# Kernel optimization log

Measured on AMD Instinct MI355X. Metric: run time of the kernel, lower is better.

Reference implementation:

```python
import jax, jax.numpy as jnp
import numpy as np

B, D, N, H = 4, 512, 1536, 8
DIM = D // H  # per-head dim = 64


def _conv1x1(x, w, b):
    # Conv1d(kernel_size=1): x [B, C, N], w [O, C], b [O]
    return jnp.einsum('oc,bcn->bon', w, x) + b[None, :, None]


def setup_inputs() -> dict:
    key = jax.random.key(0)
    ks = jax.random.split(key, 13)
    s = 0.02
    return {
        'query': jax.random.normal(ks[0], (B, D, N), jnp.float32),
        'key': jax.random.normal(ks[1], (B, D, N), jnp.float32),
        'value': jax.random.normal(ks[2], (B, D, N), jnp.float32),
        'dist': jax.random.uniform(ks[3], (B, N, N), jnp.float32),
        'mask': jax.random.bernoulli(ks[4], 0.9, (N, N)),  # bool [N, M]
        'Wq': jax.random.normal(ks[5], (D, D), jnp.float32) * s,
        'bq': jnp.zeros((D,), jnp.float32),
        'Wk': jax.random.normal(ks[6], (D, D), jnp.float32) * s,
        'bk': jnp.zeros((D,), jnp.float32),
        'Wv': jax.random.normal(ks[7], (D, D), jnp.float32) * s,
        'bv': jnp.zeros((D,), jnp.float32),
        'Wm': jax.random.normal(ks[8], (D, D), jnp.float32) * s,
        'bm': jnp.zeros((D,), jnp.float32),
    }


def reference(query, key, value, dist, mask, Wq, bq, Wk, bk, Wv, bv, Wm, bm):
    # dist is accepted but unused, exactly as in the original forward.
    q = _conv1x1(query, Wq, bq).reshape(B, DIM, H, N)
    k = _conv1x1(key, Wk, bk).reshape(B, DIM, H, N)
    v = _conv1x1(value, Wv, bv).reshape(B, DIM, H, N)
    scores = jnp.einsum('bdhn,bdhm->bhnm', q, k) / jnp.sqrt(jnp.float32(DIM))
    # custom additive mask: (detached global min - 20) on masked-out positions
    pen = (jax.lax.stop_gradient(scores.min()) - 20.0) * (~mask).astype(scores.dtype)
    scores = scores + pen[None, None]  # broadcast over [B, H]
    prob = jax.nn.softmax(scores, axis=-1)
    x = jnp.einsum('bhnm,bdhm->bdhn', prob, v).reshape(B, D, N)
    out = _conv1x1(x, Wm, bm)
    return out, scores.mean(axis=1)
```

## Files before the change

### kernel.cpp

```cpp
#include <hip/hip_runtime.h>
#include <hip/hip_bf16.h>

typedef __hip_bfloat16 bf16;
typedef __attribute__((ext_vector_type(8))) short s16x8;
typedef __attribute__((ext_vector_type(4))) float f32x4;
typedef unsigned char uchar;

#define B_   4
#define D_   512
#define N_   1536
#define H_   8
#define DIM_ 64
#define NN_  (N_*N_)

#define MFMA(a,b,c) __builtin_amdgcn_mfma_f32_16x16x32_bf16((a),(b),(c),0,0,0)

__device__ __forceinline__ short b16(float x){ bf16 h = __float2bfloat16(x); return *reinterpret_cast<short*>(&h); }
__device__ __forceinline__ float f16f(short s){ bf16 h = *reinterpret_cast<bf16*>(&s); return __bfloat162float(h); }

__device__ __forceinline__ s16x8 w8(const float* p){
  float4 u = *(const float4*)p, v = *(const float4*)(p+4);
  s16x8 r;
  r[0]=b16(u.x); r[1]=b16(u.y); r[2]=b16(u.z); r[3]=b16(u.w);
  r[4]=b16(v.x); r[5]=b16(v.y); r[6]=b16(v.z); r[7]=b16(v.w);
  return r;
}

__device__ unsigned detect_w4(const uchar* __restrict__ mraw, int* sh, int t){
  if (t == 0){ sh[0] = 0; sh[1] = 0; }
  __syncthreads();
  int a = 0, bb = 0;
  for (int i = t; i < 4096; i += 256){
    uchar v = mraw[i];
    if (v > 1) a = 1;
    else if (v && (i & 3)) bb = 1;
  }
  if (a)  atomicOr(&sh[0], 1);
  if (bb) atomicOr(&sh[1], 1);
  __syncthreads();
  return sh[0] ? 1u : (sh[1] ? 0u : 1u);
}

__global__ void detect_k(const uchar* __restrict__ mraw, unsigned* __restrict__ flags){
  __shared__ int sh[2];
  unsigned w4 = detect_w4(mraw, sh, threadIdx.x);
  if (threadIdx.x == 0) flags[0] = w4;
}

__global__ __launch_bounds__(256) void cvtW_k(const float* __restrict__ W0, const float* __restrict__ W1,
                                              const float* __restrict__ W2, const float* __restrict__ W3,
                                              bf16* __restrict__ dst){
  const float* src = (blockIdx.y==0)?W0:(blockIdx.y==1)?W1:(blockIdx.y==2)?W2:W3;
  bf16* d = dst + (size_t)blockIdx.y*(D_*D_);
  int i = (blockIdx.x*256 + threadIdx.x)*4;
  float4 v = *(const float4*)(src + i);
  __align__(8) short tmp[4] = {b16(v.x), b16(v.y), b16(v.z), b16(v.w)};
  *(int2*)((short*)d + i) = *(const int2*)tmp;
}

__device__ __forceinline__ void load_mt(uchar (*mt)[64], const void* mraw, unsigned w4,
                                        int n0, int m0, int t){
  int row = t >> 2, c = (t & 3) * 16;
  if (!w4){
    *(int4*)&mt[row][c] = *(const int4*)((const uchar*)mraw + (size_t)(n0 + row)*N_ + m0 + c);
  } else {
    const unsigned* mp = (const unsigned*)mraw + (size_t)(n0 + row)*N_ + m0 + c;
    uchar tmp[16];
    #pragma unroll
    for (int j = 0; j < 16; ++j) tmp[j] = mp[j] ? 1 : 0;
    *(int4*)&mt[row][c] = *(const int4*)tmp;
  }
}

__device__ __forceinline__ int mask_at(const void* mraw, unsigned w4, int n, int m){
  if (w4) return ((const unsigned*)mraw)[(size_t)n*N_ + m] != 0;
  return ((const uchar*)mraw)[(size_t)n*N_ + m] != 0;
}

template<int WBF>
__global__ __launch_bounds__(256) void convQKf_k(const float* __restrict__ X, const float* __restrict__ Wf,
                                                 const bf16* __restrict__ Wb,
                                                 const float* __restrict__ bias, bf16* __restrict__ dst,
                                                 float scale){
  int b = blockIdx.z, ot = blockIdx.y, nt = blockIdx.x;
  int t = threadIdx.x, w = t >> 6, L = t & 63, g = L >> 4, q = L & 15;
  __shared__ short Xs[64][72];
  __shared__ short tile[64][72];
  f32x4 acc[4] = {};
  float4 pf[4];
  #pragma unroll
  for (int it = 0; it < 4; ++it){
    int i = it*256 + t, cc = i >> 4, nq = (i & 15)*4;
    pf[it] = *(const float4*)(X + ((size_t)b*D_ + cc)*N_ + nt*64 + nq);
  }
  for (int cs = 0; cs < 8; ++cs){
    __syncthreads();
    #pragma unroll
    for (int it = 0; it < 4; ++it){
      int i = it*256 + t, cc = i >> 4, nq = (i & 15)*4;
      Xs[nq+0][cc] = b16(pf[it].x); Xs[nq+1][cc] = b16(pf[it].y);
      Xs[nq+2][cc] = b16(pf[it].z); Xs[nq+3][cc] = b16(pf[it].w);
    }
    if (cs < 7){
      #pragma unroll
      for (int it = 0; it < 4; ++it){
        int i = it*256 + t, cc = i >> 4, nq = (i & 15)*4;
        pf[it] = *(const float4*)(X + ((size_t)b*D_ + (cs+1)*64 + cc)*N_ + nt*64 + nq);
      }
    }
    __syncthreads();
    #pragma unroll
    for (int kk = 0; kk < 64; kk += 32){
      s16x8 a = *(const s16x8*)&Xs[w*16 + q][kk + 8*g];
      #pragma unroll
      for (int f = 0; f < 4; ++f){
        s16x8 bb;
        if (WBF) bb = *(const s16x8*)(Wb + (size_t)(ot*64 + f*16 + q)*D_ + cs*64 + kk + 8*g);
        else     bb = w8(Wf + (size_t)(ot*64 + f*16 + q)*D_ + cs*64 + kk + 8*g);
        acc[f] = MFMA(a, bb, acc[f]);
      }
    }
  }
  #pragma unroll
  for (int f = 0; f < 4; ++f){
    float bv = bias[ot*64 + f*16 + q];
    #pragma unroll
    for (int r = 0; r < 4; ++r)
      tile[w*16 + 4*g + r][f*16 + q] = b16((acc[f][r] + bv)*scale);
  }
  __syncthreads();
  #pragma unroll
  for (int it = 0; it < 2; ++it){
    int s = t + 256*it, row = s >> 3, h = s & 7;
    short tmp[8];
    #pragma unroll
    for (int j = 0; j < 8; ++j) tmp[j] = tile[row][h + 8*j];
    *(int4*)((short*)dst + ((size_t)(b*8+h)*N_ + nt*64 + row)*DIM_ + ot*8) = *(const int4*)tmp;
  }
}

template<int WBF>
__global__ __launch_bounds__(256) void convVf_k(const float* __restrict__ X, const float* __restrict__ Wf,
                                                const bf16* __restrict__ Wb,
                                                const float* __restrict__ bias, bf16* __restrict__ dst){
  int b = blockIdx.z, ot = blockIdx.y, nt = blockIdx.x;
  int t = threadIdx.x, w = t >> 6, L = t & 63, g = L >> 4, q = L & 15;
  __shared__ short Xs[64][72];
  __shared__ short tile[64][72];
  f32x4 acc[4] = {};
  float4 pf[4];
  #pragma unroll
  for (int it = 0; it < 4; ++it){
    int i = it*256 + t, cc = i >> 4, nq = (i & 15)*4;
    pf[it] = *(const float4*)(X + ((size_t)b*D_ + cc)*N_ + nt*64 + nq);
  }
  for (int cs = 0; cs < 8; ++cs){
    __syncthreads();
    #pragma unroll
    for (int it = 0; it < 4; ++it){
      int i = it*256 + t, cc = i >> 4, nq = (i & 15)*4;
      Xs[nq+0][cc] = b16(pf[it].x); Xs[nq+1][cc] = b16(pf[it].y);
      Xs[nq+2][cc] = b16(pf[it].z); Xs[nq+3][cc] = b16(pf[it].w);
    }
    if (cs < 7){
      #pragma unroll
      for (int it = 0; it < 4; ++it){
        int i = it*256 + t, cc = i >> 4, nq = (i & 15)*4;
        pf[it] = *(const float4*)(X + ((size_t)b*D_ + (cs+1)*64 + cc)*N_ + nt*64 + nq);
      }
    }
    __syncthreads();
    #pragma unroll
    for (int kk = 0; kk < 64; kk += 32){
      s16x8 a = *(const s16x8*)&Xs[w*16 + q][kk + 8*g];
      #pragma unroll
      for (int f = 0; f < 4; ++f){
        s16x8 bb;
        if (WBF) bb = *(const s16x8*)(Wb + (size_t)(ot*64 + f*16 + q)*D_ + cs*64 + kk + 8*g);
        else     bb = w8(Wf + (size_t)(ot*64 + f*16 + q)*D_ + cs*64 + kk + 8*g);
        acc[f] = MFMA(a, bb, acc[f]);
      }
    }
  }
  #pragma unroll
  for (int f = 0; f < 4; ++f){
    float bv = bias[ot*64 + f*16 + q];
    #pragma unroll
    for (int r = 0; r < 4; ++r)
      tile[w*16 + 4*g + r][f*16 + q] = b16(acc[f][r] + bv);
  }
  __syncthreads();
  int col = t & 63, seg = t >> 6;
  int h = col & 7, d = ot*8 + (col >> 3);
  short tmp[16];
  #pragma unroll
  for (int j = 0; j < 16; ++j) tmp[j] = tile[seg*16 + j][col];
  short* p = (short*)dst + ((size_t)(b*8+h)*DIM_ + d)*N_ + nt*64 + seg*16;
  *(int4*)p       = *(const int4*)&tmp[0];
  *(int4*)(p + 8) = *(const int4*)&tmp[8];
}

__global__ __launch_bounds__(256) void passA_k(const bf16* __restrict__ QH, const bf16* __restrict__ KH,
                                               float* __restrict__ out2f, float* __restrict__ bmin){
  int b = blockIdx.z, ntb = blockIdx.y, mtb = blockIdx.x;
  int t = threadIdx.x, w = t >> 6, L = t & 63, g = L >> 4, q = L & 15;
  __shared__ short Ks[2][64][72];
  int r0 = t >> 3, s0 = (t & 7)*8, r1 = (t + 256) >> 3;
  f32x4 mean[4] = {};
  float vmin = 3.4e38f;
  {
    const bf16* kb = KH + ((size_t)(b*H_)*N_ + mtb*64)*DIM_;
    *(int4*)&Ks[0][r0][s0] = *(const int4*)(kb + (size_t)r0*DIM_ + s0);
    *(int4*)&Ks[0][r1][s0] = *(const int4*)(kb + (size_t)r1*DIM_ + s0);
  }
  const bf16* qrow0 = QH + ((size_t)(b*H_)*N_ + ntb*64 + w*16 + q)*DIM_;
  s16x8 qa0 = *(const s16x8*)(qrow0 + 8*g);
  s16x8 qa1 = *(const s16x8*)(qrow0 + 32 + 8*g);
  int4 kn0, kn1; s16x8 qn0, qn1;
  {
    const bf16* kb = KH + ((size_t)(b*H_ + 1)*N_ + mtb*64)*DIM_;
    kn0 = *(const int4*)(kb + (size_t)r0*DIM_ + s0);
    kn1 = *(const int4*)(kb + (size_t)r1*DIM_ + s0);
    const bf16* qrow = QH + ((size_t)(b*H_ + 1)*N_ + ntb*64 + w*16 + q)*DIM_;
    qn0 = *(const s16x8*)(qrow + 8*g);
    qn1 = *(const s16x8*)(qrow + 32 + 8*g);
  }
  __syncthreads();
  for (int h = 0; h < H_; ++h){
    f32x4 acc[4] = {};
    #pragma unroll
    for (int f = 0; f < 4; ++f){
      acc[f] = MFMA(qa0, *(const s16x8*)&Ks[h&1][f*16 + q][8*g], acc[f]);
      acc[f] = MFMA(qa1, *(const s16x8*)&Ks[h&1][f*16 + q][32 + 8*g], acc[f]);
    }
    if (h < H_-1){
      *(int4*)&Ks[(h+1)&1][r0][s0] = kn0;
      *(int4*)&Ks[(h+1)&1][r1][s0] = kn1;
      qa0 = qn0; qa1 = qn1;
      if (h < H_-2){
        const bf16* kb = KH + ((size_t)(b*H_ + h+2)*N_ + mtb*64)*DIM_;
        kn0 = *(const int4*)(kb + (size_t)r0*DIM_ + s0);
        kn1 = *(const int4*)(kb + (size_t)r1*DIM_ + s0);
        const bf16* qrow = QH + ((size_t)(b*H_ + h+2)*N_ + ntb*64 + w*16 + q)*DIM_;
        qn0 = *(const s16x8*)(qrow + 8*g);
        qn1 = *(const s16x8*)(qrow + 32 + 8*g);
      }
    }
    #pragma unroll
    for (int f = 0; f < 4; ++f){
      #pragma unroll
      for (int r = 0; r < 4; ++r) vmin = fminf(vmin, acc[f][r]);
      mean[f] += acc[f];
    }
    __syncthreads();
  }
  #pragma unroll
  for (int off = 32; off; off >>= 1) vmin = fminf(vmin, __shfl_xor(vmin, off));
  __shared__ float wmin[4];
  if (L == 0) wmin[w] = vmin;
  __syncthreads();
  if (t == 0)
    bmin[((size_t)b*24 + ntb)*24 + mtb] = fminf(fminf(wmin[0],wmin[1]), fminf(wmin[2],wmin[3]));
  #pragma unroll
  for (int f = 0; f < 4; ++f)
    #pragma unroll
    for (int r = 0; r < 4; ++r)
      out2f[(size_t)b*NN_ + (size_t)(ntb*64 + w*16 + 4*g + r)*N_ + mtb*64 + f*16 + q]
        = mean[f][r] * 0.125f;
}

__global__ void minred_k(const float* __restrict__ bmin, float* __restrict__ penp){
  int t = threadIdx.x;
  float m = 3.4e38f;
  for (int i = t; i < 2304; i += 256) m = fminf(m, bmin[i]);
  #pragma unroll
  for (int off = 32; off; off >>= 1) m = fminf(m, __shfl_xor(m, off));
  __shared__ float wm[4];
  if ((t & 63) == 0) wm[t >> 6] = m;
  __syncthreads();
  if (t == 0) penp[0] = fminf(fminf(wm[0],wm[1]), fminf(wm[2],wm[3])) - 20.0f;
}

__global__ __launch_bounds__(256) void passCf_k(const void* __restrict__ mraw,
                                                const unsigned* __restrict__ flags,
                                                const float* __restrict__ penp,
                                                float* __restrict__ out2f){
  int i = blockIdx.x*256 + threadIdx.x;
  if (i >= NN_) return;
  int keep = flags[0] ? (((const unsigned*)mraw)[i] != 0) : (((const uchar*)mraw)[i] != 0);
  if (keep) return;
  float pen = penp[0];
  #pragma unroll
  for (int b = 0; b < B_; ++b) out2f[(size_t)b*NN_ + i] += pen;
}

__global__ __launch_bounds__(256) void passBs_k(const bf16* __restrict__ QH, const bf16* __restrict__ KH,
                                                const bf16* __restrict__ VT, const void* __restrict__ mraw,
                                                const unsigned* __restrict__ flags,
                                                bf16* __restrict__ Opart, float* __restrict__ lpart){
  int z = blockIdx.z, half = z >> 2, b = z & 3;
  int h = blockIdx.y, ntb = blockIdx.x;
  int t = threadIdx.x, w = t >> 6, L = t & 63, g = L >> 4, q = L & 15;
  __shared__ short Ks[64][72], Vs[64][72];
  __shared__ uchar mt[64][64];
  __shared__ short P[4][16][72];
  unsigned w4 = flags[0];
  size_t bh = (size_t)(b*H_ + h);
  const bf16* kbase = KH + bh*N_*DIM_;
  const bf16* vbase = VT + bh*(size_t)DIM_*N_;
  const bf16* qrow = QH + (bh*N_ + ntb*64 + w*16 + q)*DIM_;
  s16x8 qa0 = *(const s16x8*)(qrow + 8*g);
  s16x8 qa1 = *(const s16x8*)(qrow + 32 + 8*g);
  int r0 = t >> 3, s0 = (t & 7)*8, r1 = (t + 256) >> 3;
  int mrow = t >> 2, mc = (t & 3)*16;
  int4 kreg0, kreg1, vreg0, vreg1, mreg4[4];
  float lacc[4] = {0.f,0.f,0.f,0.f};
  f32x4 O[4] = {};
  int mt0 = half*12;
  {
    int m0 = mt0*64;
    kreg0 = *(const int4*)(kbase + (size_t)(m0 + r0)*DIM_ + s0);
    kreg1 = *(const int4*)(kbase + (size_t)(m0 + r1)*DIM_ + s0);
    vreg0 = *(const int4*)(vbase + (size_t)r0*N_ + m0 + s0);
    vreg1 = *(const int4*)(vbase + (size_t)r1*N_ + m0 + s0);
    if (!w4) mreg4[0] = *(const int4*)((const uchar*)mraw + (size_t)(ntb*64 + mrow)*N_ + m0 + mc);
    else {
      const int4* mp = (const int4*)((const unsigned*)mraw + (size_t)(ntb*64 + mrow)*N_ + m0 + mc);
      #pragma unroll
      for (int j = 0; j < 4; ++j) mreg4[j] = mp[j];
    }
  }
  for (int i = 0; i < 12; ++i){
    __syncthreads();
    *(int4*)&Ks[r0][s0] = kreg0;
    *(int4*)&Ks[r1][s0] = kreg1;
    *(int4*)&Vs[r0][s0] = vreg0;
    *(int4*)&Vs[r1][s0] = vreg1;
    if (!w4) *(int4*)&mt[mrow][mc] = mreg4[0];
    else {
      uchar tmp[16];
      #pragma unroll
      for (int j = 0; j < 16; ++j) tmp[j] = ((const unsigned*)mreg4)[j] ? 1 : 0;
      *(int4*)&mt[mrow][mc] = *(const int4*)tmp;
    }
    if (i < 11){
      int m0 = (mt0 + i + 1)*64;
      kreg0 = *(const int4*)(kbase + (size_t)(m0 + r0)*DIM_ + s0);
      kreg1 = *(const int4*)(kbase + (size_t)(m0 + r1)*DIM_ + s0);
      vreg0 = *(const int4*)(vbase + (size_t)r0*N_ + m0 + s0);
      vreg1 = *(const int4*)(vbase + (size_t)r1*N_ + m0 + s0);
      if (!w4) mreg4[0] = *(const int4*)((const uchar*)mraw + (size_t)(ntb*64 + mrow)*N_ + m0 + mc);
      else {
        const int4* mp = (const int4*)((const unsigned*)mraw + (size_t)(ntb*64 + mrow)*N_ + m0 + mc);
        #pragma unroll
        for (int j = 0; j < 4; ++j) mreg4[j] = mp[j];
      }
    }
    __syncthreads();
    f32x4 acc[4] = {};
    #pragma unroll
    for (int f = 0; f < 4; ++f){
      acc[f] = MFMA(qa0, *(const s16x8*)&Ks[f*16 + q][8*g], acc[f]);
      acc[f] = MFMA(qa1, *(const s16x8*)&Ks[f*16 + q][32 + 8*g], acc[f]);
    }
    float pv[4][4];
    #pragma unroll
    for (int f = 0; f < 4; ++f)
      #pragma unroll
      for (int r = 0; r < 4; ++r)
        pv[f][r] = mt[w*16 + 4*g + r][f*16 + q] ? __expf(acc[f][r]) : 0.0f;
    #pragma unroll
    for (int r = 0; r < 4; ++r)
      lacc[r] += (pv[0][r] + pv[1][r]) + (pv[2][r] + pv[3][r]);
    #pragma unroll
    for (int f = 0; f < 4; ++f)
      #pragma unroll
      for (int r = 0; r < 4; ++r)
        P[w][4*g + r][f*16 + q] = b16(pv[f][r]);
    #pragma unroll
    for (int f2 = 0; f2 < 4; ++f2){
      O[f2] = MFMA(*(const s16x8*)&P[w][q][8*g],      *(const s16x8*)&Vs[f2*16 + q][8*g],      O[f2]);
      O[f2] = MFMA(*(const s16x8*)&P[w][q][32 + 8*g], *(const s16x8*)&Vs[f2*16 + q][32 + 8*g], O[f2]);
    }
  }
  #pragma unroll
  for (int r = 0; r < 4; ++r){
    #pragma unroll
    for (int off = 1; off < 16; off <<= 1) lacc[r] += __shfl_xor(lacc[r], off);
  }
  bf16* Op = Opart + (size_t)half*((size_t)B_*H_*N_*DIM_);
  float* lp = lpart + (size_t)half*((size_t)B_*H_*N_);
  if (q == 0){
    #pragma unroll
    for (int r = 0; r < 4; ++r)
      lp[bh*N_ + ntb*64 + w*16 + 4*g + r] = lacc[r];
  }
  #pragma unroll
  for (int f2 = 0; f2 < 4; ++f2)
    #pragma unroll
    for (int r = 0; r < 4; ++r){
      int n = ntb*64 + w*16 + 4*g + r, d = f2*16 + q;
      ((short*)Op)[(bh*N_ + n)*DIM_ + d] = b16(O[f2][r]);
    }
}

__global__ __launch_bounds__(256) void merge_k(const bf16* __restrict__ Opart, const float* __restrict__ lpart,
                                               bf16* __restrict__ xT){
  int b = blockIdx.z, h = blockIdx.y, nt = blockIdx.x, t = threadIdx.x;
  int nl = t >> 3, d0 = (t & 7)*8;
  int n = nt*32 + nl;
  size_t bh = (size_t)(b*H_ + h);
  size_t row = bh*N_ + n;
  const size_t OS = (size_t)B_*H_*N_*DIM_, LS = (size_t)B_*H_*N_;
  float inv = 1.0f / (lpart[row] + lpart[LS + row]);
  int4 a = *(const int4*)((const short*)Opart + row*DIM_ + d0);
  int4 c = *(const int4*)((const short*)Opart + OS*1 + row*DIM_ + d0);
  const short* as = (const short*)&a;
  const short* cs = (const short*)&c;
  short* out = (short*)xT + ((size_t)b*N_ + n)*D_ + h;
  #pragma unroll
  for (int j = 0; j < 8; ++j)
    out[(size_t)(d0 + j)*8] = b16((f16f(as[j]) + f16f(cs[j])) * inv);
}

__global__ __launch_bounds__(256) void passB_k(const bf16* __restrict__ QH, const bf16* __restrict__ KH,
                                               const bf16* __restrict__ VT, const void* __restrict__ mraw,
                                               bf16* __restrict__ xT){
  int b = blockIdx.z, h = blockIdx.y, ntb = blockIdx.x;
  int t = threadIdx.x, w = t >> 6, L = t & 63, g = L >> 4, q = L & 15;
  __shared__ short Ks[64][72], Vs[64][72];
  __shared__ uchar mt[64][64];
  __shared__ short P[4][16][72];
  __shared__ int dsh[2];
  unsigned w4 = detect_w4((const uchar*)mraw, dsh, t);
  size_t bh = (size_t)(b*H_ + h);
  const bf16* kbase = KH + bh*N_*DIM_;
  const bf16* vbase = VT + bh*(size_t)DIM_*N_;
  const bf16* qrow = QH + (bh*N_ + ntb*64 + w*16 + q)*DIM_;
  s16x8 qa0 = *(const s16x8*)(qrow + 8*g);
  s16x8 qa1 = *(const s16x8*)(qrow + 32 + 8*g);
  int r0 = t >> 3, s0 = (t & 7)*8, r1 = (t + 256) >> 3;
  int mrow = t >> 2, mc = (t & 3)*16;
  int4 kreg0, kreg1, vreg0, vreg1, mreg4[4];
  float lacc[4] = {0.f,0.f,0.f,0.f};
  f32x4 O[4] = {};
  {
    kreg0 = *(const int4*)(kbase + (size_t)r0*DIM_ + s0);
    kreg1 = *(const int4*)(kbase + (size_t)r1*DIM_ + s0);
    vreg0 = *(const int4*)(vbase + (size_t)r0*N_ + s0);
    vreg1 = *(const int4*)(vbase + (size_t)r1*N_ + s0);
    if (!w4) mreg4[0] = *(const int4*)((const uchar*)mraw + (size_t)(ntb*64 + mrow)*N_ + mc);
    else {
      const int4* mp = (const int4*)((const unsigned*)mraw + (size_t)(ntb*64 + mrow)*N_ + mc);
      #pragma unroll
      for (int j = 0; j < 4; ++j) mreg4[j] = mp[j];
    }
  }
  for (int mtb = 0; mtb < 24; ++mtb){
    __syncthreads();
    *(int4*)&Ks[r0][s0] = kreg0;
    *(int4*)&Ks[r1][s0] = kreg1;
    *(int4*)&Vs[r0][s0] = vreg0;
    *(int4*)&Vs[r1][s0] = vreg1;
    if (!w4) *(int4*)&mt[mrow][mc] = mreg4[0];
    else {
      uchar tmp[16];
      #pragma unroll
      for (int j = 0; j < 16; ++j) tmp[j] = ((const unsigned*)mreg4)[j] ? 1 : 0;
      *(int4*)&mt[mrow][mc] = *(const int4*)tmp;
    }
    if (mtb < 23){
      int m0 = (mtb+1)*64;
      kreg0 = *(const int4*)(kbase + (size_t)(m0 + r0)*DIM_ + s0);
      kreg1 = *(const int4*)(kbase + (size_t)(m0 + r1)*DIM_ + s0);
      vreg0 = *(const int4*)(vbase + (size_t)r0*N_ + m0 + s0);
      vreg1 = *(const int4*)(vbase + (size_t)r1*N_ + m0 + s0);
      if (!w4) mreg4[0] = *(const int4*)((const uchar*)mraw + (size_t)(ntb*64 + mrow)*N_ + m0 + mc);
      else {
        const int4* mp = (const int4*)((const unsigned*)mraw + (size_t)(ntb*64 + mrow)*N_ + m0 + mc);
        #pragma unroll
        for (int j = 0; j < 4; ++j) mreg4[j] = mp[j];
      }
    }
    __syncthreads();
    f32x4 acc[4] = {};
    #pragma unroll
    for (int f = 0; f < 4; ++f){
      acc[f] = MFMA(qa0, *(const s16x8*)&Ks[f*16 + q][8*g], acc[f]);
      acc[f] = MFMA(qa1, *(const s16x8*)&Ks[f*16 + q][32 + 8*g], acc[f]);
    }
    float pv[4][4];
    #pragma unroll
    for (int f = 0; f < 4; ++f)
      #pragma unroll
      for (int r = 0; r < 4; ++r)
        pv[f][r] = mt[w*16 + 4*g + r][f*16 + q] ? __expf(acc[f][r]) : 0.0f;
    #pragma unroll
    for (int r = 0; r < 4; ++r)
      lacc[r] += (pv[0][r] + pv[1][r]) + (pv[2][r] + pv[3][r]);
    #pragma unroll
    for (int f = 0; f < 4; ++f)
      #pragma unroll
      for (int r = 0; r < 4; ++r)
        P[w][4*g + r][f*16 + q] = b16(pv[f][r]);
    #pragma unroll
    for (int f2 = 0; f2 < 4; ++f2){
      O[f2] = MFMA(*(const s16x8*)&P[w][q][8*g],      *(const s16x8*)&Vs[f2*16 + q][8*g],      O[f2]);
      O[f2] = MFMA(*(const s16x8*)&P[w][q][32 + 8*g], *(const s16x8*)&Vs[f2*16 + q][32 + 8*g], O[f2]);
    }
  }
  #pragma unroll
  for (int r = 0; r < 4; ++r){
    #pragma unroll
    for (int off = 1; off < 16; off <<= 1) lacc[r] += __shfl_xor(lacc[r], off);
  }
  float inv[4];
  #pragma unroll
  for (int r = 0; r < 4; ++r) inv[r] = 1.0f / lacc[r];
  #pragma unroll
  for (int f2 = 0; f2 < 4; ++f2)
    #pragma unroll
    for (int r = 0; r < 4; ++r){
      int n = ntb*64 + w*16 + 4*g + r, d = f2*16 + q;
      ((short*)xT)[((size_t)b*N_ + n)*D_ + d*8 + h] = b16(O[f2][r]*inv[r]);
    }
}

template<int WBF>
__global__ __launch_bounds__(256) void gemm2_k(const float* __restrict__ Wmf, const bf16* __restrict__ Wmb,
                                               const float* __restrict__ bm,
                                               const bf16* __restrict__ xT, float* __restrict__ out0f){
  int b = blockIdx.z, ot = blockIdx.y, nt = blockIdx.x;
  int t = threadIdx.x, w = t >> 6, L = t & 63, g = L >> 4, q = L & 15;
  f32x4 acc[4] = {};
  for (int kk = 0; kk < D_; kk += 32){
    s16x8 a;
    if (WBF) a = *(const s16x8*)(Wmb + (size_t)(ot*64 + w*16 + q)*D_ + kk + 8*g);
    else     a = w8(Wmf + (size_t)(ot*64 + w*16 + q)*D_ + kk + 8*g);
    #pragma unroll
    for (int f = 0; f < 4; ++f){
      s16x8 bb = *(const s16x8*)(xT + ((size_t)b*N_ + nt*64 + f*16 + q)*D_ + kk + 8*g);
      acc[f] = MFMA(a, bb, acc[f]);
    }
  }
  #pragma unroll
  for (int f = 0; f < 4; ++f)
    #pragma unroll
    for (int r = 0; r < 4; ++r){
      int o = ot*64 + w*16 + 4*g + r;
      out0f[((size_t)b*D_ + o)*N_ + nt*64 + f*16 + q] = acc[f][r] + bm[o];
    }
}

__global__ __launch_bounds__(256) void t64_k(const float* __restrict__ X, bf16* __restrict__ XT){
  int b = blockIdx.z, ct = blockIdx.y, nt = blockIdx.x, t = threadIdx.x;
  __shared__ bf16 T[64][72];
  #pragma unroll
  for (int it = 0; it < 4; ++it){
    int idx = t + 256*it, cc = idx >> 4, s = idx & 15;
    float4 v = *(const float4*)(X + ((size_t)b*D_ + ct*64 + cc)*N_ + nt*64 + s*4);
    T[cc][s*4+0] = __float2bfloat16(v.x);
    T[cc][s*4+1] = __float2bfloat16(v.y);
    T[cc][s*4+2] = __float2bfloat16(v.z);
    T[cc][s*4+3] = __float2bfloat16(v.w);
  }
  __syncthreads();
  #pragma unroll
  for (int it = 0; it < 2; ++it){
    int idx = t + 256*it, nn = idx >> 3, s = idx & 7;
    short tmp[8];
    #pragma unroll
    for (int j = 0; j < 8; ++j) tmp[j] = *(short*)&T[s*8 + j][nn];
    *(int4*)((short*)XT + ((size_t)b*N_ + nt*64 + nn)*D_ + ct*64 + s*8) = *(const int4*)tmp;
  }
}

__global__ __launch_bounds__(256) void convQK_k(const bf16* __restrict__ XT, const float* __restrict__ W,
                                                const float* __restrict__ bias, bf16* __restrict__ dst,
                                                float scale){
  int b = blockIdx.z, ot = blockIdx.y, nt = blockIdx.x;
  int t = threadIdx.x, w = t >> 6, L = t & 63, g = L >> 4, q = L & 15;
  const bf16* Arow = XT + ((size_t)b*N_ + nt*64 + w*16 + q)*D_;
  f32x4 acc[4] = {};
  for (int kk = 0; kk < D_; kk += 32){
    s16x8 a = *(const s16x8*)(Arow + kk + 8*g);
    #pragma unroll
    for (int f = 0; f < 4; ++f){
      s16x8 bb = w8(W + (size_t)(ot*64 + f*16 + q)*D_ + kk + 8*g);
      acc[f] = MFMA(a, bb, acc[f]);
    }
  }
  __shared__ short tile[64][72];
  #pragma unroll
  for (int f = 0; f < 4; ++f){
    float bv = bias[ot*64 + f*16 + q];
    #pragma unroll
    for (int r = 0; r < 4; ++r)
      tile[w*16 + 4*g + r][f*16 + q] = b16((acc[f][r] + bv)*scale);
  }
  __syncthreads();
  #pragma unroll
  for (int it = 0; it < 2; ++it){
    int s = t + 256*it, row = s >> 3, h = s & 7;
    short tmp[8];
    #pragma unroll
    for (int j = 0; j < 8; ++j) tmp[j] = tile[row][h + 8*j];
    *(int4*)((short*)dst + ((size_t)(b*8+h)*N_ + nt*64 + row)*DIM_ + ot*8) = *(const int4*)tmp;
  }
}

__global__ __launch_bounds__(256) void convV_k(const bf16* __restrict__ XT, const float* __restrict__ W,
                                               const float* __restrict__ bias, bf16* __restrict__ dst){
  int b = blockIdx.z, ot = blockIdx.y, nt = blockIdx.x;
  int t = threadIdx.x, w = t >> 6, L = t & 63, g = L >> 4, q = L & 15;
  const bf16* Arow = XT + ((size_t)b*N_ + nt*64 + w*16 + q)*D_;
  f32x4 acc[4] = {};
  for (int kk = 0; kk < D_; kk += 32){
    s16x8 a = *(const s16x8*)(Arow + kk + 8*g);
    #pragma unroll
    for (int f = 0; f < 4; ++f){
      s16x8 bb = w8(W + (size_t)(ot*64 + f*16 + q)*D_ + kk + 8*g);
      acc[f] = MFMA(a, bb, acc[f]);
    }
  }
  __shared__ short tile[64][72];
  #pragma unroll
  for (int f = 0; f < 4; ++f){
    float bv = bias[ot*64 + f*16 + q];
    #pragma unroll
    for (int r = 0; r < 4; ++r)
      tile[w*16 + 4*g + r][f*16 + q] = b16(acc[f][r] + bv);
  }
  __syncthreads();
  int col = t & 63, seg = t >> 6;
  int h = col & 7, d = ot*8 + (col >> 3);
  short tmp[16];
  #pragma unroll
  for (int j = 0; j < 16; ++j) tmp[j] = tile[seg*16 + j][col];
  short* p = (short*)dst + ((size_t)(b*8+h)*DIM_ + d)*N_ + nt*64 + seg*16;
  *(int4*)p       = *(const int4*)&tmp[0];
  *(int4*)(p + 8) = *(const int4*)&tmp[8];
}

__global__ __launch_bounds__(256) void min_k(const bf16* __restrict__ QH, const bf16* __restrict__ KH,
                                             float* __restrict__ bmin){
  int b = blockIdx.z, ntb = blockIdx.y, mtb = blockIdx.x;
  int t = threadIdx.x, w = t >> 6, L = t & 63, g = L >> 4, q = L & 15;
  float vmin = 3.4e38f;
  for (int h = 0; h < H_; ++h){
    size_t bh = (size_t)(b*H_ + h);
    const bf16* qrow = QH + (bh*N_ + ntb*64 + w*16 + q)*DIM_;
    const bf16* krow = KH + (bh*N_ + mtb*64 + q)*DIM_;
    f32x4 acc[4] = {};
    #pragma unroll
    for (int kk = 0; kk < 64; kk += 32){
      s16x8 a = *(const s16x8*)(qrow + kk + 8*g);
      #pragma unroll
      for (int f = 0; f < 4; ++f){
        s16x8 bb = *(const s16x8*)(krow + (size_t)f*16*DIM_ + kk + 8*g);
        acc[f] = MFMA(a, bb, acc[f]);
      }
    }
    #pragma unroll
    for (int f = 0; f < 4; ++f)
      #pragma unroll
      for (int r = 0; r < 4; ++r) vmin = fminf(vmin, acc[f][r]);
  }
  #pragma unroll
  for (int off = 32; off; off >>= 1) vmin = fminf(vmin, __shfl_xor(vmin, off));
  __shared__ float wmin[4];
  if (L == 0) wmin[w] = vmin;
  __syncthreads();
  if (t == 0)
    bmin[((size_t)b*24 + ntb)*24 + mtb] = fminf(fminf(wmin[0],wmin[1]), fminf(wmin[2],wmin[3]));
}

__global__ __launch_bounds__(256) void meanLow_k(const bf16* __restrict__ QH, const bf16* __restrict__ KH,
                                                 const void* __restrict__ mraw, const float* __restrict__ penp,
                                                 float* __restrict__ out2f){
  int mtb = blockIdx.x, rt = blockIdx.y;
  if (rt == 48 && mtb == 0) return;
  __shared__ uchar mt[64][64];
  __shared__ int dsh[2];
  int t = threadIdx.x, w = t >> 6, L = t & 63, g = L >> 4, q = L & 15;
  unsigned w4 = detect_w4((const uchar*)mraw, dsh, t);
  int gr = rt*64, b = gr / N_, n0 = gr % N_;
  load_mt(mt, mraw, w4, n0, mtb*64, t);
  __syncthreads();
  float pen = penp[0];
  f32x4 mean[4] = {};
  for (int h = 0; h < H_; ++h){
    size_t bh = (size_t)(b*H_ + h);
    const bf16* qrow = QH + (bh*N_ + n0 + w*16 + q)*DIM_;
    const bf16* krow = KH + (bh*N_ + mtb*64 + q)*DIM_;
    f32x4 acc[4] = {};
    #pragma unroll
    for (int kk = 0; kk < 64; kk += 32){
      s16x8 a = *(const s16x8*)(qrow + kk + 8*g);
      #pragma unroll
      for (int f = 0; f < 4; ++f){
        s16x8 bb = *(const s16x8*)(krow + (size_t)f*16*DIM_ + kk + 8*g);
        acc[f] = MFMA(a, bb, acc[f]);
      }
    }
    #pragma unroll
    for (int f = 0; f < 4; ++f) mean[f] += acc[f];
  }
  #pragma unroll
  for (int f = 0; f < 4; ++f)
    #pragma unroll
    for (int r = 0; r < 4; ++r){
      float v = mean[f][r]*0.125f;
      if (!mt[w*16 + 4*g + r][f*16 + q]) v += pen;
      out2f[(size_t)b*NN_ + (size_t)(n0 + w*16 + 4*g + r)*N_ + mtb*64 + f*16 + q] = v;
    }
}

__device__ void build_head(const float* __restrict__ X, const float* __restrict__ W,
                           const float* __restrict__ bias, int b, int n0, int h,
                           short (*dst)[72], short (*Xs)[72], int t){
  int w = t >> 6, L = t & 63, g = L >> 4, q = L & 15;
  f32x4 acc[4] = {};
  for (int cs = 0; cs < 8; ++cs){
    __syncthreads();
    #pragma unroll
    for (int it = 0; it < 4; ++it){
      int i = it*256 + t, cc = i >> 4, nq = (i & 15)*4;
      float4 v = *(const float4*)(X + ((size_t)b*D_ + cs*64 + cc)*N_ + n0 + nq);
      Xs[nq+0][cc] = b16(v.x); Xs[nq+1][cc] = b16(v.y);
      Xs[nq+2][cc] = b16(v.z); Xs[nq+3][cc] = b16(v.w);
    }
    __syncthreads();
    #pragma unroll
    for (int kk = 0; kk < 64; kk += 32){
      s16x8 a = w8(W + (size_t)((w*16 + q)*8 + h)*D_ + cs*64 + kk + 8*g);
      #pragma unroll
      for (int f = 0; f < 4; ++f){
        s16x8 bb = *(const s16x8*)&Xs[f*16 + q][kk + 8*g];
        acc[f] = MFMA(a, bb, acc[f]);
      }
    }
  }
  __syncthreads();
  #pragma unroll
  for (int f = 0; f < 4; ++f)
    #pragma unroll
    for (int r = 0; r < 4; ++r){
      int d = w*16 + 4*g + r, n = f*16 + q;
      dst[n][d] = b16(acc[f][r] + bias[d*8 + h]);
    }
  __syncthreads();
}

__global__ __launch_bounds__(256) void meanHigh_k(const float* __restrict__ Xq, const float* __restrict__ Wq,
                                                  const float* __restrict__ bq,
                                                  const float* __restrict__ Xk, const float* __restrict__ Wk,
                                                  const float* __restrict__ bk,
                                                  const void* __restrict__ mraw, const float* __restrict__ penp,
                                                  float* __restrict__ out2f){
  __shared__ short qt[64][72], kt[64][72], Xs[64][72];
  __shared__ int dsh[2];
  int t = threadIdx.x, w = t >> 6, L = t & 63, g = L >> 4, q = L & 15;
  unsigned w4 = detect_w4((const uchar*)mraw, dsh, t);
  int rt = 64 + blockIdx.y, gr = rt*64, b = gr / N_, n0 = gr % N_;
  float pen = penp[0];
  f32x4 mean[6][4] = {};
  for (int h = 0; h < H_; ++h){
    build_head(Xq, Wq, bq, b, n0, h, qt, Xs, t);
    for (int mi = 0; mi < 6; ++mi){
      int m0 = (blockIdx.x*6 + mi)*64;
      build_head(Xk, Wk, bk, b, m0, h, kt, Xs, t);
      f32x4 acc[4] = {};
      #pragma unroll
      for (int kk = 0; kk < 64; kk += 32){
        s16x8 a = *(const s16x8*)&qt[w*16 + q][kk + 8*g];
        #pragma unroll
        for (int f = 0; f < 4; ++f){
          s16x8 bb = *(const s16x8*)&kt[f*16 + q][kk + 8*g];
          acc[f] = MFMA(a, bb, acc[f]);
        }
      }
      #pragma unroll
      for (int f = 0; f < 4; ++f) mean[mi][f] += acc[f]*0.125f;
    }
  }
  for (int mi = 0; mi < 6; ++mi){
    int m0 = (blockIdx.x*6 + mi)*64;
    #pragma unroll
    for (int f = 0; f < 4; ++f)
      #pragma unroll
      for (int r = 0; r < 4; ++r){
        int n = n0 + w*16 + 4*g + r, m = m0 + f*16 + q;
        float v = mean[mi][f][r]*0.125f;
        if (!mask_at(mraw, w4, n, m)) v += pen;
        out2f[(size_t)b*NN_ + (size_t)n*N_ + m] = v;
      }
  }
}

__global__ __launch_bounds__(256) void meanFinal_k(const float* __restrict__ Xq, const float* __restrict__ Wq,
                                                   const float* __restrict__ bq,
                                                   const float* __restrict__ Xk, const float* __restrict__ Wk,
                                                   const float* __restrict__ bk,
                                                   const void* __restrict__ mraw, const float* __restrict__ penp,
                                                   float* __restrict__ out2f){
  __shared__ short qt[64][72], kt[64][72], Xs[64][72];
  __shared__ int dsh[2];
  int t = threadIdx.x, w = t >> 6, L = t & 63, g = L >> 4, q = L & 15;
  unsigned w4 = detect_w4((const uchar*)mraw, dsh, t);
  float pen = penp[0];
  const int b = 2, n0 = 0, m0 = 0;
  f32x4 mean[4] = {};
  for (int h = 0; h < H_; ++h){
    build_head(Xq, Wq, bq, b, n0, h, qt, Xs, t);
    build_head(Xk, Wk, bk, b, m0, h, kt, Xs, t);
    f32x4 acc[4] = {};
    #pragma unroll
    for (int kk = 0; kk < 64; kk += 32){
      s16x8 a = *(const s16x8*)&qt[w*16 + q][kk + 8*g];
      #pragma unroll
      for (int f = 0; f < 4; ++f){
        s16x8 bb = *(const s16x8*)&kt[f*16 + q][kk + 8*g];
        acc[f] = MFMA(a, bb, acc[f]);
      }
    }
    #pragma unroll
    for (int f = 0; f < 4; ++f) mean[f] += acc[f]*0.125f;
  }
  #pragma unroll
  for (int f = 0; f < 4; ++f)
    #pragma unroll
    for (int r = 0; r < 4; ++r){
      int n = n0 + w*16 + 4*g + r, m = m0 + f*16 + q;
      float v = mean[f][r]*0.125f;
      if (!mask_at(mraw, w4, n, m)) v += pen;
      out2f[(size_t)b*NN_ + (size_t)n*N_ + m] = v;
    }
}

extern "C" void kernel_launch(void* const* d_in, const int* in_sizes, int n_in,
                              void* d_out, int out_size, void* d_ws, size_t ws_size,
                              hipStream_t stream) {
  (void)in_sizes; (void)n_in; (void)out_size;
  const float* query = (const float*)d_in[0];
  const float* key   = (const float*)d_in[1];
  const float* value = (const float*)d_in[2];
  const void*  mraw  = d_in[4];
  const float* Wq = (const float*)d_in[5],  *bq = (const float*)d_in[6];
  const float* Wk = (const float*)d_in[7],  *bk = (const float*)d_in[8];
  const float* Wv = (const float*)d_in[9],  *bv = (const float*)d_in[10];
  const float* Wm = (const float*)d_in[11], *bm = (const float*)d_in[12];

  const size_t E = (size_t)B_*D_*N_;
  float* out0f = (float*)d_out;
  float* out2f = out0f + E;
  char*  base  = (char*)d_out;

  const size_t WB      = (size_t)4*D_*D_*sizeof(bf16);
  const size_t LPART   = (size_t)2*B_*H_*N_*sizeof(float);
  const size_t needF   = 16384 + 4*E;
  const size_t needF2  = 16384 + WB + 4*E;
  const size_t needF3  = needF2 + LPART;

  if (ws_size >= needF){
    const bool wbf   = (ws_size >= needF2);
    const bool split = (ws_size >= needF3);
    char* ws = (char*)d_ws;
    unsigned* flags = (unsigned*)ws;
    float* penp = (float*)(ws + 64);
    float* bmin = (float*)(ws + 256);
    bf16* Wb  = (bf16*)(ws + 16384);
    bf16* S_Q = wbf ? (bf16*)(ws + 16384 + WB) : (bf16*)(ws + 16384);
    bf16* S_K = S_Q + E;
    float* lpart = (float*)((char*)(S_K + E));
    bf16* S_V = (bf16*)(base + 8*E);
    bf16* S_X = (bf16*)(base + 10*E);
    bf16* Opart = (bf16*)(base + 12*E);

    detect_k<<<1, 256, 0, stream>>>((const uchar*)mraw, flags);

    if (wbf){
      cvtW_k<<<dim3(D_*D_/1024, 4), 256, 0, stream>>>(Wq, Wk, Wv, Wm, Wb);
      convQKf_k<1><<<dim3(24,8,B_), 256, 0, stream>>>(query, Wq, Wb,                   bq, S_Q, 0.125f);
      convQKf_k<1><<<dim3(24,8,B_), 256, 0, stream>>>(key,   Wk, Wb + (size_t)D_*D_,   bk, S_K, 1.0f);
      convVf_k <1><<<dim3(24,8,B_), 256, 0, stream>>>(value, Wv, Wb + (size_t)2*D_*D_, bv, S_V);
    } else {
      convQKf_k<0><<<dim3(24,8,B_), 256, 0, stream>>>(query, Wq, nullptr, bq, S_Q, 0.125f);
      convQKf_k<0><<<dim3(24,8,B_), 256, 0, stream>>>(key,   Wk, nullptr, bk, S_K, 1.0f);
      convVf_k <0><<<dim3(24,8,B_), 256, 0, stream>>>(value, Wv, nullptr, bv, S_V);
    }

    if (split){
      passBs_k<<<dim3(24,8,8), 256, 0, stream>>>(S_Q, S_K, S_V, mraw, flags, Opart, lpart);
      merge_k <<<dim3(48,8,B_), 256, 0, stream>>>(Opart, lpart, S_X);
    } else {
      passB_k <<<dim3(24,8,B_), 256, 0, stream>>>(S_Q, S_K, S_V, mraw, S_X);
    }
    if (wbf) gemm2_k<1><<<dim3(24,8,B_), 256, 0, stream>>>(Wm, Wb + (size_t)3*D_*D_, bm, S_X, out0f);
    else     gemm2_k<0><<<dim3(24,8,B_), 256, 0, stream>>>(Wm, nullptr,              bm, S_X, out0f);

    passA_k <<<dim3(24,24,B_), 256, 0, stream>>>(S_Q, S_K, out2f, bmin);
    minred_k<<<1, 256, 0, stream>>>(bmin, penp);
    passCf_k<<<NN_/256, 256, 0, stream>>>(mraw, flags, penp, out2f);
  } else {
    bf16* S_V = (bf16*)(base + 8*E);
    bf16* S_X = (bf16*)(base + 10*E);
    bf16* S_Q = (bf16*)(base + 12*E);
    bf16* S_K = (bf16*)(base + 14*E);
    float* penp = (float*)S_X;
    float* bmin = (float*)(base + 10*E + 256);

    t64_k   <<<dim3(24,8,B_), 256, 0, stream>>>(query, S_X);
    convQK_k<<<dim3(24,8,B_), 256, 0, stream>>>(S_X, Wq, bq, S_Q, 0.125f);
    t64_k   <<<dim3(24,8,B_), 256, 0, stream>>>(key, S_X);
    convQK_k<<<dim3(24,8,B_), 256, 0, stream>>>(S_X, Wk, bk, S_K, 1.0f);
    t64_k   <<<dim3(24,8,B_), 256, 0, stream>>>(value, S_X);
    convV_k <<<dim3(24,8,B_), 256, 0, stream>>>(S_X, Wv, bv, S_V);

    passB_k <<<dim3(24,8,B_), 256, 0, stream>>>(S_Q, S_K, S_V, mraw, S_X);
    gemm2_k<0><<<dim3(24,8,B_), 256, 0, stream>>>(Wm, nullptr, bm, S_X, out0f);

    min_k   <<<dim3(24,24,B_), 256, 0, stream>>>(S_Q, S_K, bmin);
    minred_k<<<1, 256, 0, stream>>>(bmin, penp);

    meanLow_k  <<<dim3(24,64), 256, 0, stream>>>(S_Q, S_K, mraw, penp, out2f);
    meanHigh_k <<<dim3(4,32),  256, 0, stream>>>(query, Wq, bq, key, Wk, bk, mraw, penp, out2f);
    meanFinal_k<<<1, 256, 0, stream>>>(query, Wq, bq, key, Wk, bk, mraw, penp, out2f);
  }
}
```

Before: 256.0 us.

## Process two 64-row query tiles per block in split attention pass

Each passBs block now handles 128 query rows, running two Q tiles against each staged K/V tile so every shared-memory K/V load is reused twice. The grid is halved to 12 blocks in x, which cuts K/V global traffic. The 4-byte mask path now reads global memory directly at store time instead of prefetching into registers. The cost is higher register use (two sets of O accumulators), fewer blocks (768) available to fill the GPU, and a serialized P buffer shared between the two sub-tiles.

```diff
diff --git a/kernel.cpp b/kernel.cpp
--- a/kernel.cpp
+++ b/kernel.cpp
@@ -302,20 +302,25 @@
   int h = blockIdx.y, ntb = blockIdx.x;
   int t = threadIdx.x, w = t >> 6, L = t & 63, g = L >> 4, q = L & 15;
   __shared__ short Ks[64][72], Vs[64][72];
-  __shared__ uchar mt[64][64];
+  __shared__ uchar mt[128][64];
   __shared__ short P[4][16][72];
   unsigned w4 = flags[0];
   size_t bh = (size_t)(b*H_ + h);
   const bf16* kbase = KH + bh*N_*DIM_;
   const bf16* vbase = VT + bh*(size_t)DIM_*N_;
-  const bf16* qrow = QH + (bh*N_ + ntb*64 + w*16 + q)*DIM_;
-  s16x8 qa0 = *(const s16x8*)(qrow + 8*g);
-  s16x8 qa1 = *(const s16x8*)(qrow + 32 + 8*g);
+  int n0 = ntb*128;
+  const bf16* qrow = QH + (bh*N_ + n0 + w*16 + q)*DIM_;
+  s16x8 qa00 = *(const s16x8*)(qrow + 8*g);
+  s16x8 qa01 = *(const s16x8*)(qrow + 32 + 8*g);
+  s16x8 qa10 = *(const s16x8*)(qrow + (size_t)64*DIM_ + 8*g);
+  s16x8 qa11 = *(const s16x8*)(qrow + (size_t)64*DIM_ + 32 + 8*g);
   int r0 = t >> 3, s0 = (t & 7)*8, r1 = (t + 256) >> 3;
-  int mrow = t >> 2, mc = (t & 3)*16;
-  int4 kreg0, kreg1, vreg0, vreg1, mreg4[4];
-  float lacc[4] = {0.f,0.f,0.f,0.f};
-  f32x4 O[4] = {};
+  int mrA = t >> 2, mcA = (t & 3)*16;
+  int mrB = 64 + (t >> 2), mcB = mcA;
+  int4 kreg0, kreg1, vreg0, vreg1;
+  int4 mregA = {}, mregB = {};
+  float lacc0[4] = {0.f,0.f,0.f,0.f}, lacc1[4] = {0.f,0.f,0.f,0.f};
+  f32x4 O0[4] = {}, O1[4] = {};
   int mt0 = half*12;
   {
     int m0 = mt0*64;
@@ -323,84 +328,124 @@
     kreg1 = *(const int4*)(kbase + (size_t)(m0 + r1)*DIM_ + s0);
     vreg0 = *(const int4*)(vbase + (size_t)r0*N_ + m0 + s0);
     vreg1 = *(const int4*)(vbase + (size_t)r1*N_ + m0 + s0);
-    if (!w4) mreg4[0] = *(const int4*)((const uchar*)mraw + (size_t)(ntb*64 + mrow)*N_ + m0 + mc);
-    else {
-      const int4* mp = (const int4*)((const unsigned*)mraw + (size_t)(ntb*64 + mrow)*N_ + m0 + mc);
-      #pragma unroll
-      for (int j = 0; j < 4; ++j) mreg4[j] = mp[j];
+    if (!w4){
+      mregA = *(const int4*)((const uchar*)mraw + (size_t)(n0 + mrA)*N_ + m0 + mcA);
+      mregB = *(const int4*)((const uchar*)mraw + (size_t)(n0 + mrB)*N_ + m0 + mcB);
     }
   }
   for (int i = 0; i < 12; ++i){
+    int m0 = (mt0 + i)*64;
     __syncthreads();
     *(int4*)&Ks[r0][s0] = kreg0;
     *(int4*)&Ks[r1][s0] = kreg1;
     *(int4*)&Vs[r0][s0] = vreg0;
     *(int4*)&Vs[r1][s0] = vreg1;
-    if (!w4) *(int4*)&mt[mrow][mc] = mreg4[0];
-    else {
-      uchar tmp[16];
-      #pragma unroll
-      for (int j = 0; j < 16; ++j) tmp[j] = ((const unsigned*)mreg4)[j] ? 1 : 0;
-      *(int4*)&mt[mrow][mc] = *(const int4*)tmp;
+    if (!w4){
+      *(int4*)&mt[mrA][mcA] = mregA;
+      *(int4*)&mt[mrB][mcB] = mregB;
+    } else {
+      #pragma unroll
+      for (int j = 0; j < 2; ++j){
+        int row = j*64 + mrA;
+        const unsigned* mp = (const unsigned*)mraw + (size_t)(n0 + row)*N_ + m0 + mcA;
+        uchar tmp[16];
+        #pragma unroll
+        for (int k2 = 0; k2 < 16; ++k2) tmp[k2] = mp[k2] ? 1 : 0;
+        *(int4*)&mt[row][mcA] = *(const int4*)tmp;
+      }
     }
     if (i < 11){
-      int m0 = (mt0 + i + 1)*64;
-      kreg0 = *(const int4*)(kbase + (size_t)(m0 + r0)*DIM_ + s0);
-      kreg1 = *(const int4*)(kbase + (size_t)(m0 + r1)*DIM_ + s0);
-      vreg0 = *(const int4*)(vbase + (size_t)r0*N_ + m0 + s0);
-      vreg1 = *(const int4*)(vbase + (size_t)r1*N_ + m0 + s0);
-      if (!w4) mreg4[0] = *(const int4*)((const uchar*)mraw + (size_t)(ntb*64 + mrow)*N_ + m0 + mc);
-      else {
-        const int4* mp = (const int4*)((const unsigned*)mraw + (size_t)(ntb*64 + mrow)*N_ + m0 + mc);
+      int m1 = (mt0 + i + 1)*64;
+      kreg0 = *(const int4*)(kbase + (size_t)(m1 + r0)*DIM_ + s0);
+      kreg1 = *(const int4*)(kbase + (size_t)(m1 + r1)*DIM_ + s0);
+      vreg0 = *(const int4*)(vbase + (size_t)r0*N_ + m1 + s0);
+      vreg1 = *(const int4*)(vbase + (size_t)r1*N_ + m1 + s0);
+      if (!w4){
+        mregA = *(const int4*)((const uchar*)mraw + (size_t)(n0 + mrA)*N_ + m1 + mcA);
+        mregB = *(const int4*)((const uchar*)mraw + (size_t)(n0 + mrB)*N_ + m1 + mcB);
+      }
+    }
+    __syncthreads();
+    {
+      f32x4 acc[4] = {};
+      #pragma unroll
+      for (int f = 0; f < 4; ++f){
+        acc[f] = MFMA(qa00, *(const s16x8*)&Ks[f*16 + q][8*g], acc[f]);
+        acc[f] = MFMA(qa01, *(const s16x8*)&Ks[f*16 + q][32 + 8*g], acc[f]);
+      }
+      float pv[4][4];
+      #pragma unroll
+      for (int f = 0; f < 4; ++f)
         #pragma unroll
-        for (int j = 0; j < 4; ++j) mreg4[j] = mp[j];
-      }
-    }
-    __syncthreads();
-    f32x4 acc[4] = {};
-    #pragma unroll
-    for (int f = 0; f < 4; ++f){
-      acc[f] = MFMA(qa0, *(const s16x8*)&Ks[f*16 + q][8*g], acc[f]);
-      acc[f] = MFMA(qa1, *(const s16x8*)&Ks[f*16 + q][32 + 8*g], acc[f]);
-    }
-    float pv[4][4];
-    #pragma unroll
-    for (int f = 0; f < 4; ++f)
+        for (int r = 0; r < 4; ++r)
+          pv[f][r] = mt[w*16 + 4*g + r][f*16 + q] ? __expf(acc[f][r]) : 0.0f;
       #pragma unroll
       for (int r = 0; r < 4; ++r)
-        pv[f][r] = mt[w*16 + 4*g + r][f*16 + q] ? __expf(acc[f][r]) : 0.0f;
-    #pragma unroll
-    for (int r = 0; r < 4; ++r)
-      lacc[r] += (pv[0][r] + pv[1][r]) + (pv[2][r] + pv[3][r]);
-    #pragma unroll
-    for (int f = 0; f < 4; ++f)
+        lacc0[r] += (pv[0][r] + pv[1][r]) + (pv[2][r] + pv[3][r]);
+      #pragma unroll
+      for (int f = 0; f < 4; ++f)
+        #pragma unroll
+        for (int r = 0; r < 4; ++r)
+          P[w][4*g + r][f*16 + q] = b16(pv[f][r]);
+      #pragma unroll
+      for (int f2 = 0; f2 < 4; ++f2){
+        O0[f2] = MFMA(*(const s16x8*)&P[w][q][8*g],      *(const s16x8*)&Vs[f2*16 + q][8*g],      O0[f2]);
+        O0[f2] = MFMA(*(const s16x8*)&P[w][q][32 + 8*g], *(const s16x8*)&Vs[f2*16 + q][32 + 8*g], O0[f2]);
+      }
+    }
+    {
+      f32x4 acc[4] = {};
+      #pragma unroll
+      for (int f = 0; f < 4; ++f){
+        acc[f] = MFMA(qa10, *(const s16x8*)&Ks[f*16 + q][8*g], acc[f]);
+        acc[f] = MFMA(qa11, *(const s16x8*)&Ks[f*16 + q][32 + 8*g], acc[f]);
+      }
+      float pv[4][4];
+      #pragma unroll
+      for (int f = 0; f < 4; ++f)
+        #pragma unroll
+        for (int r = 0; r < 4; ++r)
+          pv[f][r] = mt[64 + w*16 + 4*g + r][f*16 + q] ? __expf(acc[f][r]) : 0.0f;
       #pragma unroll
       for (int r = 0; r < 4; ++r)
-        P[w][4*g + r][f*16 + q] = b16(pv[f][r]);
-    #pragma unroll
-    for (int f2 = 0; f2 < 4; ++f2){
-      O[f2] = MFMA(*(const s16x8*)&P[w][q][8*g],      *(const s16x8*)&Vs[f2*16 + q][8*g],      O[f2]);
-      O[f2] = MFMA(*(const s16x8*)&P[w][q][32 + 8*g], *(const s16x8*)&Vs[f2*16 + q][32 + 8*g], O[f2]);
+        lacc1[r] += (pv[0][r] + pv[1][r]) + (pv[2][r] + pv[3][r]);
+      #pragma unroll
+      for (int f = 0; f < 4; ++f)
+        #pragma unroll
+        for (int r = 0; r < 4; ++r)
+          P[w][4*g + r][f*16 + q] = b16(pv[f][r]);
+      #pragma unroll
+      for (int f2 = 0; f2 < 4; ++f2){
+        O1[f2] = MFMA(*(const s16x8*)&P[w][q][8*g],      *(const s16x8*)&Vs[f2*16 + q][8*g],      O1[f2]);
+        O1[f2] = MFMA(*(const s16x8*)&P[w][q][32 + 8*g], *(const s16x8*)&Vs[f2*16 + q][32 + 8*g], O1[f2]);
+      }
     }
   }
   #pragma unroll
   for (int r = 0; r < 4; ++r){
     #pragma unroll
-    for (int off = 1; off < 16; off <<= 1) lacc[r] += __shfl_xor(lacc[r], off);
+    for (int off = 1; off < 16; off <<= 1){
+      lacc0[r] += __shfl_xor(lacc0[r], off);
+      lacc1[r] += __shfl_xor(lacc1[r], off);
+    }
   }
   bf16* Op = Opart + (size_t)half*((size_t)B_*H_*N_*DIM_);
   float* lp = lpart + (size_t)half*((size_t)B_*H_*N_);
   if (q == 0){
     #pragma unroll
-    for (int r = 0; r < 4; ++r)
-      lp[bh*N_ + ntb*64 + w*16 + 4*g + r] = lacc[r];
+    for (int r = 0; r < 4; ++r){
+      lp[bh*N_ + n0 + w*16 + 4*g + r]      = lacc0[r];
+      lp[bh*N_ + n0 + 64 + w*16 + 4*g + r] = lacc1[r];
+    }
   }
   #pragma unroll
   for (int f2 = 0; f2 < 4; ++f2)
     #pragma unroll
     for (int r = 0; r < 4; ++r){
-      int n = ntb*64 + w*16 + 4*g + r, d = f2*16 + q;
-      ((short*)Op)[(bh*N_ + n)*DIM_ + d] = b16(O[f2][r]);
+      int d = f2*16 + q;
+      int na = n0 + w*16 + 4*g + r;
+      ((short*)Op)[(bh*N_ + na)*DIM_ + d]      = b16(O0[f2][r]);
+      ((short*)Op)[(bh*N_ + na + 64)*DIM_ + d] = b16(O1[f2][r]);
     }
 }
 
@@ -891,7 +936,7 @@
     }
 
     if (split){
-      passBs_k<<<dim3(24,8,8), 256, 0, stream>>>(S_Q, S_K, S_V, mraw, flags, Opart, lpart);
+      passBs_k<<<dim3(12,8,8), 256, 0, stream>>>(S_Q, S_K, S_V, mraw, flags, Opart, lpart);
       merge_k <<<dim3(48,8,B_), 256, 0, stream>>>(Opart, lpart, S_X);
     } else {
       passB_k <<<dim3(24,8,B_), 256, 0, stream>>>(S_Q, S_K, S_V, mraw, S_X);
```

New measurement: 268.7 us. 4.9% more time.
